# Performance work log

Measured on AMD Instinct MI355X. Metric: run time of the kernel, lower is better.

## Reference

```python
import jax, jax.numpy as jnp
import numpy as np

NUM_SEGMENTS = 128  # batch_size * alpha_iter


def setup_inputs() -> dict:
    key = jax.random.key(0)
    ks = jax.random.split(key, 16)
    T, E, H, C, O = 131072, 256, 512, 256, 32
    words = jax.random.normal(ks[0], (T, E), dtype=jnp.float32)
    seg_ids = jnp.sort(jax.random.randint(ks[1], (T,), 0, NUM_SEGMENTS))
    def lin(kw, kb, fi, fo):
        s = 1.0 / np.sqrt(fi)
        return (jax.random.uniform(kw, (fi, fo), minval=-s, maxval=s, dtype=jnp.float32),
                jax.random.uniform(kb, (fo,), minval=-s, maxval=s, dtype=jnp.float32))
    W1, b1 = lin(ks[2], ks[3], E, H)
    W2, b2 = lin(ks[4], ks[5], H, H)
    W3, b3 = lin(ks[6], ks[7], H, C)
    P1, pb1 = lin(ks[8], ks[9], C, H)
    P2, pb2 = lin(ks[10], ks[11], H, H)
    P3, pb3 = lin(ks[12], ks[13], H, O)
    return {"words": words, "seg_ids": seg_ids,
            "W1": W1, "b1": b1, "W2": W2, "b2": b2, "W3": W3, "b3": b3,
            "P1": P1, "pb1": pb1, "P2": P2, "pb2": pb2, "P3": P3, "pb3": pb3,
            "batch_size": 16, "alpha_iter": 8}


def reference(words, seg_ids, W1, b1, W2, b2, W3, b3,
              P1, pb1, P2, pb2, P3, pb3, batch_size, alpha_iter):
    # encoder MLP on every token: Linear-tanh-Linear-tanh-Linear
    h = jnp.tanh(words @ W1 + b1)
    h = jnp.tanh(h @ W2 + b2)
    tok_enc = h @ W3 + b3                                  # [T, enc_dim]
    # per-set sum pooling (ragged sum over each word tensor)
    enc = jax.ops.segment_sum(tok_enc, seg_ids, num_segments=batch_size * alpha_iter)
    # predictor MLP
    p = jnp.tanh(enc @ P1 + pb1)
    p = jnp.tanh(p @ P2 + pb2)
    pred = p @ P3 + pb3                                    # [B*A, target_dim]
    return pred.reshape(batch_size, alpha_iter, -1)
```

## Files before the change

### kernel.cpp

```cpp
#include <hip/hip_runtime.h>
#include <hip/hip_bf16.h>
#include <hip/hip_fp16.h>


typedef _Float16 half8v __attribute__((ext_vector_type(8)));
typedef _Float16 half4v __attribute__((ext_vector_type(4)));
typedef float f32x4 __attribute__((ext_vector_type(4)));
typedef float f32x16 __attribute__((ext_vector_type(16)));

#define TANH_SCALE 2.8853900817779268f
#define A_STR 1032
#define E_STRF 129

__global__ __launch_bounds__(256) void wt_kernel(
    const float* __restrict__ W1, const float* __restrict__ W2,
    const float* __restrict__ W3,
    _Float16* __restrict__ F1, _Float16* __restrict__ F2,
    _Float16* __restrict__ F3) {
    int u = blockIdx.x * 256 + threadIdx.x;
    const float* W; _Float16* F; int FW, NFT, u0; float scale;
    if (u < 16384)      { W = W1; F = F1; FW = 512; NFT = 16; u0 = u;         scale = TANH_SCALE; }
    else if (u < 49152) { W = W2; F = F2; FW = 512; NFT = 16; u0 = u - 16384; scale = TANH_SCALE; }
    else                { W = W3; F = F3; FW = 256; NFT = 8;  u0 = u - 49152; scale = 1.0f; }
    int lane = u0 & 63, frag = u0 >> 6;
    int ft = frag % NFT, ks = frag / NFT;
    int f = ft * 32 + (lane & 31);
    int k0 = ks * 16 + (lane >> 5) * 8;
    half8v v;
    #pragma unroll
    for (int j = 0; j < 8; ++j)
        v[j] = (_Float16)(W[(size_t)(k0 + j) * FW + f] * scale);
    *(half8v*)((char*)F + (size_t)u0 * 16) = v;
}

__device__ __forceinline__ half8v read_b(const char* p, int off) {
    uint2 lo = *(const uint2*)(p + off);
    uint2 hi = *(const uint2*)(p + off + 8);
    uint4 w;
    w.x = lo.x; w.y = lo.y; w.z = hi.x; w.w = hi.y;
    return __builtin_bit_cast(half8v, w);
}

template<int K, int MT, int NT, int NFT>
__device__ __forceinline__ void mlp_pass32(const char* __restrict__ F, int wave,
                                           const char* lds_act,
                                           const float* sbias_layer, int lane,
                                           f32x16 acc[MT][NT]) {
    const int r2 = lane & 31;
    const int hi = lane >> 5;
    const int fbase = wave * (MT * 32);
    #pragma unroll
    for (int mt = 0; mt < MT; ++mt)
        #pragma unroll
        for (int q = 0; q < 4; ++q) {
            f32x4 bv = *(const f32x4*)(sbias_layer + fbase + mt * 32 + hi * 4 + q * 8);
            #pragma unroll
            for (int nt = 0; nt < NT; ++nt)
                #pragma unroll
                for (int j = 0; j < 4; ++j) acc[mt][nt][q * 4 + j] = bv[j];
        }
    const char* fb = F + ((size_t)wave * MT) * 1024 + lane * 16;
    const char* bb = lds_act + r2 * A_STR + hi * 16;

    constexpr int NS = K / 16;
    half8v A[3][MT], B[2][NT];
    #pragma unroll
    for (int mt = 0; mt < MT; ++mt) {
        A[0][mt] = *(const half8v*)(fb + mt * 1024);
        A[1][mt] = *(const half8v*)(fb + (NFT + mt) * 1024);
    }
    #pragma unroll
    for (int nt = 0; nt < NT; ++nt)
        B[0][nt] = read_b(bb, nt * 32 * A_STR);

    #pragma unroll
    for (int s = 0; s < NS; ++s) {
        if (s + 2 < NS) {
            #pragma unroll
            for (int mt = 0; mt < MT; ++mt)
                A[(s + 2) % 3][mt] =
                    *(const half8v*)(fb + ((size_t)(s + 2) * NFT + mt) * 1024);
        }
        if (s + 1 < NS) {
            #pragma unroll
            for (int nt = 0; nt < NT; ++nt)
                B[(s + 1) & 1][nt] = read_b(bb, nt * 32 * A_STR + (s + 1) * 32);
        }
        #pragma unroll
        for (int nt = 0; nt < NT; ++nt)
            #pragma unroll
            for (int mt = 0; mt < MT; ++mt)
                acc[mt][nt] = __builtin_amdgcn_mfma_f32_32x32x16_f16(
                    A[s % 3][mt], B[s & 1][nt], acc[mt][nt], 0, 0, 0);
    }
}

template<int MT, int NT>
__device__ __forceinline__ void store_h32(char* lds_out, const f32x16 acc[MT][NT],
                                          int fbase, int lane) {
    const int t_lo = lane & 31;
    const int hi = lane >> 5;
    #pragma unroll
    for (int mt = 0; mt < MT; ++mt)
        #pragma unroll
        for (int nt = 0; nt < NT; ++nt) {
            int t = nt * 32 + t_lo;
            #pragma unroll
            for (int q = 0; q < 4; ++q) {
                int f0 = fbase + mt * 32 + hi * 4 + q * 8;
                half4v hv;
                #pragma unroll
                for (int j = 0; j < 4; ++j) {
                    float e = __builtin_amdgcn_exp2f(acc[mt][nt][q * 4 + j]);
                    float rr = __builtin_amdgcn_rcpf(e + 1.0f);
                    hv[j] = (_Float16)fmaf(-2.0f, rr, 1.0f);
                }
                *(half4v*)(lds_out + t * A_STR + f0 * 2) = hv;
            }
        }
}

__global__ __launch_bounds__(512, 2) void encoder_kernel(
    const float* __restrict__ words, const int* __restrict__ seg_ids,
    const _Float16* __restrict__ F1, const _Float16* __restrict__ F2,
    const _Float16* __restrict__ F3,
    const float* __restrict__ b1, const float* __restrict__ b2,
    const float* __restrict__ b3, float* __restrict__ enc) {
    __shared__ __align__(16) char buf[132096];
    __shared__ __align__(16) float sbias[1280];
    __shared__ int sseg[128];

    const int tid = threadIdx.x;
    const int lane = tid & 63;
    const int wave = tid >> 6;
    const int tok0 = blockIdx.x * 128;

    sbias[tid] = b1[tid] * TANH_SCALE;
    sbias[512 + tid] = b2[tid] * TANH_SCALE;
    if (tid < 256) sbias[1024 + tid] = b3[tid];
    if (tid < 128) sseg[tid] = seg_ids[tok0 + tid];

    const float* wsrc = words + (size_t)tok0 * 256;
    #pragma unroll
    for (int it = 0; it < 16; ++it) {
        int i = it * 512 + tid;
        float4 v = ((const float4*)wsrc)[i];
        int t = i >> 6;
        int col = i & 63;
        half4v hv = { (_Float16)v.x, (_Float16)v.y, (_Float16)v.z, (_Float16)v.w };
        *(half4v*)(buf + t * A_STR + col * 8) = hv;
    }
    __syncthreads();

    {
        f32x16 acc[2][4];
        mlp_pass32<256, 2, 4, 16>((const char*)F1, wave, buf, sbias, lane, acc);
        __syncthreads();
        store_h32<2, 4>(buf, acc, wave * 64, lane);
    }
    __syncthreads();

    {
        f32x16 acc[2][4];
        mlp_pass32<512, 2, 4, 16>((const char*)F2, wave, buf, sbias + 512, lane, acc);
        __syncthreads();
        store_h32<2, 4>(buf, acc, wave * 64, lane);
    }
    __syncthreads();

    {
        f32x16 acc[1][4];
        mlp_pass32<512, 1, 4, 8>((const char*)F3, wave, buf, sbias + 1024, lane, acc);
        __syncthreads();
        float* encT = (float*)buf;
        const int t_lo = lane & 31;
        const int hi = lane >> 5;
        #pragma unroll
        for (int nt = 0; nt < 4; ++nt) {
            int t = nt * 32 + t_lo;
            #pragma unroll
            for (int q = 0; q < 4; ++q) {
                int f0 = wave * 32 + hi * 4 + q * 8;
                #pragma unroll
                for (int j = 0; j < 4; ++j)
                    encT[(f0 + j) * E_STRF + t] = acc[0][nt][q * 4 + j];
            }
        }
    }
    __syncthreads();

    {
        int f = tid & 255;
        int hh = tid >> 8;
        int t0 = hh * 64;
        const float* encT = (const float*)buf;
        float a = 0.0f;
        int cur = sseg[t0];
        for (int i = 0; i < 64; ++i) {
            int t = t0 + i;
            float v = encT[f * E_STRF + t];
            int s = sseg[t];
            if (s != cur) { atomicAdd(&enc[cur * 256 + f], a); a = 0.0f; cur = s; }
            a += v;
        }
        atomicAdd(&enc[cur * 256 + f], a);
    }
}

__global__ __launch_bounds__(256) void pred_kernel(
    const float* __restrict__ enc,
    const float* __restrict__ P1, const float* __restrict__ pb1,
    const float* __restrict__ P2, const float* __restrict__ pb2,
    const float* __restrict__ P3, const float* __restrict__ pb3,
    float* __restrict__ out) {
    __shared__ float se[256];
    __shared__ float sp[512];
    __shared__ float red[256];
    const int tid = threadIdx.x, b = blockIdx.x;
    se[tid] = enc[b * 256 + tid];
    __syncthreads();
    float a0 = pb1[tid], a1 = pb1[tid + 256];
    for (int k = 0; k < 256; ++k) {
        float e = se[k];
        a0 = fmaf(e, P1[k * 512 + tid], a0);
        a1 = fmaf(e, P1[k * 512 + tid + 256], a1);
    }
    sp[tid] = tanhf(a0);
    sp[tid + 256] = tanhf(a1);
    __syncthreads();
    a0 = pb2[tid]; a1 = pb2[tid + 256];
    for (int k = 0; k < 512; ++k) {
        float p = sp[k];
        a0 = fmaf(p, P2[k * 512 + tid], a0);
        a1 = fmaf(p, P2[k * 512 + tid + 256], a1);
    }
    __syncthreads();
    sp[tid] = tanhf(a0);
    sp[tid + 256] = tanhf(a1);
    __syncthreads();
    int j = tid & 31, part = tid >> 5;
    float s = 0.0f;
    for (int k = part * 64; k < part * 64 + 64; ++k)
        s = fmaf(sp[k], P3[k * 32 + j], s);
    red[tid] = s;
    __syncthreads();
    if (tid < 128) red[tid] += red[tid + 128];
    __syncthreads();
    if (tid < 64) red[tid] += red[tid + 64];
    __syncthreads();
    if (tid < 32) out[b * 32 + tid] = red[tid] + red[tid + 32] + pb3[tid];
}

extern "C" void kernel_launch(void* const* d_in, const int* in_sizes, int n_in,
                              void* d_out, int out_size, void* d_ws, size_t ws_size,
                              hipStream_t stream) {
    const float* words = (const float*)d_in[0];
    const int* seg_ids = (const int*)d_in[1];
    const float* W1 = (const float*)d_in[2];
    const float* b1 = (const float*)d_in[3];
    const float* W2 = (const float*)d_in[4];
    const float* b2 = (const float*)d_in[5];
    const float* W3 = (const float*)d_in[6];
    const float* b3 = (const float*)d_in[7];
    const float* P1 = (const float*)d_in[8];
    const float* pb1 = (const float*)d_in[9];
    const float* P2 = (const float*)d_in[10];
    const float* pb2 = (const float*)d_in[11];
    const float* P3 = (const float*)d_in[12];
    const float* pb3 = (const float*)d_in[13];
    float* out = (float*)d_out;

    char* ws = (char*)d_ws;
    _Float16* F1 = (_Float16*)(ws);
    _Float16* F2 = (_Float16*)(ws + 262144);
    _Float16* F3 = (_Float16*)(ws + 786432);
    float* enc = (float*)(ws + 1048576);

    hipMemsetAsync(enc, 0, 128 * 256 * 4, stream);
    wt_kernel<<<256, 256, 0, stream>>>(W1, W2, W3, F1, F2, F3);
    encoder_kernel<<<1024, 512, 0, stream>>>(words, seg_ids, F1, F2, F3,
                                             b1, b2, b3, enc);
    pred_kernel<<<128, 256, 0, stream>>>(enc, P1, pb1, P2, pb2, P3, pb3, out);
}
```

Measured before the change: 248.8 us.

## Use 1024-thread encoder blocks with one feature tile per wave

Doubles the encoder block to 16 waves with one block per CU. Each wave now computes a single 32-feature MFMA tile instead of two, and layer 3 splits work across both feature and token halves. The aim is more resident waves per CU to hide latency and fewer accumulators per wave. In exchange each weight fragment read is shared across fewer MFMAs, and a single block per CU loses overlap between blocks at the barriers.

```diff
diff --git a/kernel.cpp b/kernel.cpp
--- a/kernel.cpp
+++ b/kernel.cpp
@@ -41,46 +41,37 @@
     return __builtin_bit_cast(half8v, w);
 }
 
-template<int K, int MT, int NT, int NFT>
-__device__ __forceinline__ void mlp_pass32(const char* __restrict__ F, int wave,
+template<int K, int NT, int NFT>
+__device__ __forceinline__ void mlp_pass32(const char* __restrict__ F,
+                                           int fragsel, int tokofs,
                                            const char* lds_act,
-                                           const float* sbias_layer, int lane,
-                                           f32x16 acc[MT][NT]) {
+                                           const float* sbias_f, int lane,
+                                           f32x16 acc[NT]) {
     const int r2 = lane & 31;
     const int hi = lane >> 5;
-    const int fbase = wave * (MT * 32);
-    #pragma unroll
-    for (int mt = 0; mt < MT; ++mt)
-        #pragma unroll
-        for (int q = 0; q < 4; ++q) {
-            f32x4 bv = *(const f32x4*)(sbias_layer + fbase + mt * 32 + hi * 4 + q * 8);
-            #pragma unroll
-            for (int nt = 0; nt < NT; ++nt)
-                #pragma unroll
-                for (int j = 0; j < 4; ++j) acc[mt][nt][q * 4 + j] = bv[j];
-        }
-    const char* fb = F + ((size_t)wave * MT) * 1024 + lane * 16;
-    const char* bb = lds_act + r2 * A_STR + hi * 16;
+    #pragma unroll
+    for (int q = 0; q < 4; ++q) {
+        f32x4 bv = *(const f32x4*)(sbias_f + hi * 4 + q * 8);
+        #pragma unroll
+        for (int nt = 0; nt < NT; ++nt)
+            #pragma unroll
+            for (int j = 0; j < 4; ++j) acc[nt][q * 4 + j] = bv[j];
+    }
+    const char* fb = F + (size_t)fragsel * 1024 + lane * 16;
+    const char* bb = lds_act + (size_t)(tokofs + r2) * A_STR + hi * 16;
 
     constexpr int NS = K / 16;
-    half8v A[3][MT], B[2][NT];
-    #pragma unroll
-    for (int mt = 0; mt < MT; ++mt) {
-        A[0][mt] = *(const half8v*)(fb + mt * 1024);
-        A[1][mt] = *(const half8v*)(fb + (NFT + mt) * 1024);
-    }
+    half8v A[3], B[2][NT];
+    A[0] = *(const half8v*)(fb);
+    A[1] = *(const half8v*)(fb + (size_t)NFT * 1024);
     #pragma unroll
     for (int nt = 0; nt < NT; ++nt)
         B[0][nt] = read_b(bb, nt * 32 * A_STR);
 
     #pragma unroll
     for (int s = 0; s < NS; ++s) {
-        if (s + 2 < NS) {
-            #pragma unroll
-            for (int mt = 0; mt < MT; ++mt)
-                A[(s + 2) % 3][mt] =
-                    *(const half8v*)(fb + ((size_t)(s + 2) * NFT + mt) * 1024);
-        }
+        if (s + 2 < NS)
+            A[(s + 2) % 3] = *(const half8v*)(fb + ((size_t)(s + 2) * NFT) * 1024);
         if (s + 1 < NS) {
             #pragma unroll
             for (int nt = 0; nt < NT; ++nt)
@@ -88,39 +79,35 @@
         }
         #pragma unroll
         for (int nt = 0; nt < NT; ++nt)
-            #pragma unroll
-            for (int mt = 0; mt < MT; ++mt)
-                acc[mt][nt] = __builtin_amdgcn_mfma_f32_32x32x16_f16(
-                    A[s % 3][mt], B[s & 1][nt], acc[mt][nt], 0, 0, 0);
-    }
-}
-
-template<int MT, int NT>
-__device__ __forceinline__ void store_h32(char* lds_out, const f32x16 acc[MT][NT],
+            acc[nt] = __builtin_amdgcn_mfma_f32_32x32x16_f16(
+                A[s % 3], B[s & 1][nt], acc[nt], 0, 0, 0);
+    }
+}
+
+template<int NT>
+__device__ __forceinline__ void store_h32(char* lds_out, const f32x16 acc[NT],
                                           int fbase, int lane) {
     const int t_lo = lane & 31;
     const int hi = lane >> 5;
     #pragma unroll
-    for (int mt = 0; mt < MT; ++mt)
-        #pragma unroll
-        for (int nt = 0; nt < NT; ++nt) {
-            int t = nt * 32 + t_lo;
-            #pragma unroll
-            for (int q = 0; q < 4; ++q) {
-                int f0 = fbase + mt * 32 + hi * 4 + q * 8;
-                half4v hv;
-                #pragma unroll
-                for (int j = 0; j < 4; ++j) {
-                    float e = __builtin_amdgcn_exp2f(acc[mt][nt][q * 4 + j]);
-                    float rr = __builtin_amdgcn_rcpf(e + 1.0f);
-                    hv[j] = (_Float16)fmaf(-2.0f, rr, 1.0f);
-                }
-                *(half4v*)(lds_out + t * A_STR + f0 * 2) = hv;
+    for (int nt = 0; nt < NT; ++nt) {
+        int t = nt * 32 + t_lo;
+        #pragma unroll
+        for (int q = 0; q < 4; ++q) {
+            int f0 = fbase + hi * 4 + q * 8;
+            half4v hv;
+            #pragma unroll
+            for (int j = 0; j < 4; ++j) {
+                float e = __builtin_amdgcn_exp2f(acc[nt][q * 4 + j]);
+                float rr = __builtin_amdgcn_rcpf(e + 1.0f);
+                hv[j] = (_Float16)fmaf(-2.0f, rr, 1.0f);
             }
-        }
-}
-
-__global__ __launch_bounds__(512, 2) void encoder_kernel(
+            *(half4v*)(lds_out + t * A_STR + f0 * 2) = hv;
+        }
+    }
+}
+
+__global__ __launch_bounds__(1024, 1) void encoder_kernel(
     const float* __restrict__ words, const int* __restrict__ seg_ids,
     const _Float16* __restrict__ F1, const _Float16* __restrict__ F2,
     const _Float16* __restrict__ F3,
@@ -135,15 +122,15 @@
     const int wave = tid >> 6;
     const int tok0 = blockIdx.x * 128;
 
-    sbias[tid] = b1[tid] * TANH_SCALE;
-    sbias[512 + tid] = b2[tid] * TANH_SCALE;
+    if (tid < 512) sbias[tid] = b1[tid] * TANH_SCALE;
+    else           sbias[tid] = b2[tid - 512] * TANH_SCALE;
     if (tid < 256) sbias[1024 + tid] = b3[tid];
     if (tid < 128) sseg[tid] = seg_ids[tok0 + tid];
 
     const float* wsrc = words + (size_t)tok0 * 256;
     #pragma unroll
-    for (int it = 0; it < 16; ++it) {
-        int i = it * 512 + tid;
+    for (int it = 0; it < 8; ++it) {
+        int i = it * 1024 + tid;
         float4 v = ((const float4*)wsrc)[i];
         int t = i >> 6;
         int col = i & 63;
@@ -153,37 +140,41 @@
     __syncthreads();
 
     {
-        f32x16 acc[2][4];
-        mlp_pass32<256, 2, 4, 16>((const char*)F1, wave, buf, sbias, lane, acc);
+        f32x16 acc[4];
+        mlp_pass32<256, 4, 16>((const char*)F1, wave, 0, buf,
+                               sbias + wave * 32, lane, acc);
         __syncthreads();
-        store_h32<2, 4>(buf, acc, wave * 64, lane);
-    }
-    __syncthreads();
-
-    {
-        f32x16 acc[2][4];
-        mlp_pass32<512, 2, 4, 16>((const char*)F2, wave, buf, sbias + 512, lane, acc);
+        store_h32<4>(buf, acc, wave * 32, lane);
+    }
+    __syncthreads();
+
+    {
+        f32x16 acc[4];
+        mlp_pass32<512, 4, 16>((const char*)F2, wave, 0, buf,
+                               sbias + 512 + wave * 32, lane, acc);
         __syncthreads();
-        store_h32<2, 4>(buf, acc, wave * 64, lane);
-    }
-    __syncthreads();
-
-    {
-        f32x16 acc[1][4];
-        mlp_pass32<512, 1, 4, 8>((const char*)F3, wave, buf, sbias + 1024, lane, acc);
+        store_h32<4>(buf, acc, wave * 32, lane);
+    }
+    __syncthreads();
+
+    {
+        const int fw = wave >> 1, tw = wave & 1;
+        f32x16 acc[2];
+        mlp_pass32<512, 2, 8>((const char*)F3, fw, tw * 64, buf,
+                              sbias + 1024 + fw * 32, lane, acc);
         __syncthreads();
         float* encT = (float*)buf;
         const int t_lo = lane & 31;
         const int hi = lane >> 5;
         #pragma unroll
-        for (int nt = 0; nt < 4; ++nt) {
-            int t = nt * 32 + t_lo;
+        for (int nt = 0; nt < 2; ++nt) {
+            int t = tw * 64 + nt * 32 + t_lo;
             #pragma unroll
             for (int q = 0; q < 4; ++q) {
-                int f0 = wave * 32 + hi * 4 + q * 8;
+                int f0 = fw * 32 + hi * 4 + q * 8;
                 #pragma unroll
                 for (int j = 0; j < 4; ++j)
-                    encT[(f0 + j) * E_STRF + t] = acc[0][nt][q * 4 + j];
+                    encT[(f0 + j) * E_STRF + t] = acc[nt][q * 4 + j];
             }
         }
     }
@@ -191,12 +182,12 @@
 
     {
         int f = tid & 255;
-        int hh = tid >> 8;
-        int t0 = hh * 64;
+        int qq = tid >> 8;
+        int t0 = qq * 32;
         const float* encT = (const float*)buf;
         float a = 0.0f;
         int cur = sseg[t0];
-        for (int i = 0; i < 64; ++i) {
+        for (int i = 0; i < 32; ++i) {
             int t = t0 + i;
             float v = encT[f * E_STRF + t];
             int s = sseg[t];
@@ -278,7 +269,7 @@
 
     hipMemsetAsync(enc, 0, 128 * 256 * 4, stream);
     wt_kernel<<<256, 256, 0, stream>>>(W1, W2, W3, F1, F2, F3);
-    encoder_kernel<<<1024, 512, 0, stream>>>(words, seg_ids, F1, F2, F3,
-                                             b1, b2, b3, enc);
+    encoder_kernel<<<1024, 1024, 0, stream>>>(words, seg_ids, F1, F2, F3,
+                                              b1, b2, b3, enc);
     pred_kernel<<<128, 256, 0, stream>>>(enc, P1, pb1, P2, pb2, P3, pb3, out);
 }
```

New measurement: 235.8 us. 1.06x faster.
